# Kernel optimization log

Measured on AMD Instinct MI355X. Metric: run time of the kernel, lower is better.

The kernel has to match this reference:

```python
import jax, jax.numpy as jnp
import numpy as np

B, T, W, D = 4, 1000, 32, 200
ED, N, DCONV, DTR = 400, 16, 4, 13  # d_inner=2*d_model, d_state, d_conv, dt_rank=ceil(200/16)


def _causal_conv(x, w, b):
    # x: (B, L, ED), depthwise causal conv, kernel DCONV
    L = x.shape[1]
    xp = jnp.pad(x, ((0, 0), (DCONV - 1, 0), (0, 0)))
    y = sum(xp[:, k:k + L, :] * w[:, k] for k in range(DCONV))
    return y + b


def _ssm(x, A_log, Dp, xproj, dtw, dtb):
    # selective scan; x: (B, L, ED)
    A = -jnp.exp(A_log)                      # (ED, N)
    dbc = x @ xproj                          # (B, L, DTR+2N)
    delta, Bm, Cm = dbc[..., :DTR], dbc[..., DTR:DTR + N], dbc[..., DTR + N:]
    dt = jax.nn.softplus(delta @ dtw + dtb)  # (B, L, ED)
    dA = jnp.exp(dt[..., None] * A)                         # (B, L, ED, N)
    dBx = dt[..., None] * Bm[:, :, None, :] * x[..., None]  # (B, L, ED, N)

    def step(h, t):
        dA_t, dBx_t, C_t = t
        h = dA_t * h + dBx_t
        y = jnp.einsum('ben,bn->be', h, C_t)
        return h, y

    h0 = jnp.zeros((x.shape[0], ED, N), x.dtype)
    xs = (dA.transpose(1, 0, 2, 3), dBx.transpose(1, 0, 2, 3), Cm.transpose(1, 0, 2))
    _, ys = jax.lax.scan(step, h0, xs)
    return ys.transpose(1, 0, 2) + Dp * x


def _branch(x, in_proj, conv_w, conv_b, xproj, dtw, dtb, A_log, Dp):
    xz = x @ in_proj
    xp, z = xz[..., :ED], xz[..., ED:]
    xp = jax.nn.silu(_causal_conv(xp, conv_w, conv_b))
    y = _ssm(xp, A_log, Dp, xproj, dtw, dtb)
    return y * jax.nn.silu(z)


def setup_inputs() -> dict:
    key = jax.random.key(0)
    ks = jax.random.split(key, 24)
    s = 0.02
    nrm = lambda k, shape: jax.random.normal(k, shape, jnp.float32) * s
    inp = {}
    inp['input_ids'] = jax.random.normal(ks[0], (B, T, W, D), jnp.float32)
    inp['n_tweets'] = jax.random.randint(ks[1], (B,), 1, T + 1)
    inp['n_words'] = jax.random.randint(ks[2], (B, T), 1, W + 1)
    inp['cls_token'] = jnp.zeros((1, 1, D), jnp.float32)
    inp['w_attn'] = nrm(ks[3], (D, 1))
    inp['b_attn'] = jnp.zeros((1,), jnp.float32)
    inp['norm_w'] = jnp.ones((D,), jnp.float32)
    for i, d in enumerate(('f', 'b')):
        o = i * 8
        inp[f'in_proj_{d}'] = nrm(ks[4 + o], (D, 2 * ED))
        inp[f'conv_w_{d}'] = nrm(ks[5 + o], (ED, DCONV))
        inp[f'conv_b_{d}'] = jnp.zeros((ED,), jnp.float32)
        inp[f'xproj_{d}'] = nrm(ks[6 + o], (ED, DTR + 2 * N))
        inp[f'dtw_{d}'] = nrm(ks[7 + o], (DTR, ED))
        inp[f'dtb_{d}'] = jnp.zeros((ED,), jnp.float32)
        inp[f'A_log_{d}'] = jnp.log(jnp.broadcast_to(jnp.arange(1, N + 1, dtype=jnp.float32), (ED, N)))
        inp[f'D_{d}'] = jnp.ones((ED,), jnp.float32)
    inp['out_proj'] = nrm(ks[20], (ED, D))
    inp['head_w'] = nrm(ks[21], (D, 1))
    inp['head_b'] = jnp.zeros((1,), jnp.float32)
    return inp


def reference(input_ids, n_tweets, n_words, cls_token, w_attn, b_attn, norm_w,
              in_proj_f, conv_w_f, conv_b_f, xproj_f, dtw_f, dtb_f, A_log_f, D_f,
              in_proj_b, conv_w_b, conv_b_b, xproj_b, dtw_b, dtb_b, A_log_b, D_b,
              out_proj, head_w, head_b):
    Bz, Tz, Wz, Dz = input_ids.shape
    # ragged per-tweet attention pooling, fully vectorized with masks
    scores = jnp.squeeze(input_ids @ w_attn, -1) + b_attn[0]        # (B, T, W)
    wmask = jnp.arange(Wz) < n_words[..., None]                     # (B, T, W)
    scores = jnp.where(wmask, scores, -jnp.inf)
    attn = jax.nn.softmax(scores, axis=-1)
    tw = jnp.einsum('btw,btwd->btd', attn, input_ids)               # (B, T, D)
    tmask = jnp.arange(Tz) < n_tweets[:, None]
    tw = jnp.where(tmask[..., None], tw, 0.0)                       # padded tweets stay zero
    pos = Tz // 2
    x = jnp.concatenate([tw[:, :pos], jnp.broadcast_to(cls_token, (Bz, 1, Dz)), tw[:, pos:]], axis=1)
    # one bidirectional Mamba layer: pre-RMSNorm residual block
    xn = x * jax.lax.rsqrt(jnp.mean(x * x, axis=-1, keepdims=True) + 1e-5) * norm_w
    y_f = _branch(xn, in_proj_f, conv_w_f, conv_b_f, xproj_f, dtw_f, dtb_f, A_log_f, D_f)
    y_b = jnp.flip(_branch(jnp.flip(xn, 1), in_proj_b, conv_w_b, conv_b_b, xproj_b, dtw_b, dtb_b, A_log_b, D_b), 1)
    x = x + (y_f + y_b) @ out_proj
    logit = jnp.squeeze(x[:, pos] @ head_w, -1) + head_b[0]
    return jax.nn.sigmoid(logit)
```

## Files before the change

kernel.cpp:

```cpp
#include <hip/hip_runtime.h>
#include <cmath>

#define Bz 4
#define Tz 1000
#define Wz 32
#define Dz 200
#define EDz 400
#define Nz 16
#define DTRz 13
#define Lz 1001
#define POSz 500
#define LPz 501
#define TSTR 512
#define NEE 7
#define NZB 8
#define ZTOT 29728
#define NEG_BIG -1e30f

__device__ __forceinline__ float wave_sum(float v) {
#pragma unroll
  for (int o = 32; o; o >>= 1) v += __shfl_xor(v, o);
  return v;
}

__global__ __launch_bounds__(256) void k_front(
    const float* __restrict__ x, const int* __restrict__ n_tweets,
    const int* __restrict__ n_words, const float* __restrict__ w_attn,
    const float* __restrict__ b_attn, const float* __restrict__ norm_w,
    const float* __restrict__ cls, const float* __restrict__ out_proj,
    const float* __restrict__ head_w, const float* __restrict__ ipf,
    const float* __restrict__ ipb, float* __restrict__ xn,
    float* __restrict__ zbuf, float* __restrict__ vbuf,
    float* __restrict__ zero_base) {
  int bid = blockIdx.x;
  int tid = threadIdx.x;
  int wave = tid >> 6, lane = tid & 63;
  if (bid < 9) {
    if (bid == 0) {
      __shared__ float hw[Dz];
      if (tid < Dz) hw[tid] = head_w[tid];
      __syncthreads();
      for (int e = tid; e < EDz; e += 256) {
        float acc = 0.f;
        for (int d = 0; d < Dz; d += 4) {
          float4 ov = *(const float4*)(out_proj + e * Dz + d);
          acc += ov.x * hw[d] + ov.y * hw[d + 1] + ov.z * hw[d + 2] + ov.w * hw[d + 3];
        }
        vbuf[e] = acc;
      }
      return;
    }
    int id = bid - 1;
    int br = id >> 2, b = id & 3;
    __shared__ float xs[Dz];
    __shared__ float s_red[4];
    float val = (tid < Dz) ? cls[tid] : 0.f;
    float sq = wave_sum(val * val);
    if ((tid & 63) == 0) s_red[tid >> 6] = sq;
    __syncthreads();
    float tot = s_red[0] + s_red[1] + s_red[2] + s_red[3];
    float scale = rsqrtf(tot * (1.f / Dz) + 1e-5f);
    if (tid < Dz) {
      float o = val * scale * norm_w[tid];
      xs[tid] = o;
      if (br == 0) xn[((size_t)b * Lz + POSz) * Dz + tid] = o;
    }
    __syncthreads();
    const float* ip = br ? ipb : ipf;
    for (int e = tid; e < EDz; e += 256) {
      float acc = 0.f;
      for (int d = 0; d < Dz; ++d) acc += xs[d] * ip[d * (2 * EDz) + EDz + e];
      zbuf[((size_t)br * Bz + b) * EDz + e] = acc;
    }
    return;
  }
  if (bid < 9 + NZB) {
    int zb = bid - 9;
    float4* z = (float4*)zero_base;
    int per = ZTOT / NZB;
    for (int i = tid; i < per; i += 256)
      z[zb * per + i] = make_float4(0.f, 0.f, 0.f, 0.f);
    return;
  }
  int bt = (bid - 9 - NZB) * 4 + wave;
  int b = bt / Tz, t = bt - b * Tz;
  int l = (t < POSz) ? t : t + 1;
  float* outr = xn + ((size_t)b * Lz + l) * Dz;
  int ntw = n_tweets[b]; if (ntw > Tz) ntw = Tz;
  if (t >= ntw) {
    if (lane < 50) *(float4*)(outr + lane * 4) = make_float4(0.f, 0.f, 0.f, 0.f);
    return;
  }
  int nw = n_words[b * Tz + t]; if (nw > Wz) nw = Wz; if (nw < 1) nw = 1;
  const float* xs = x + ((size_t)(b * Tz + t)) * (Wz * Dz);
  int h = lane & 1, w = lane >> 1;
  float sc = 0.f;
  if (w < nw) {
    const float* xr = xs + w * Dz + h * 100;
    const float* wr = w_attn + h * 100;
#pragma unroll
    for (int i = 0; i < 25; ++i) {
      float4 xv = *(const float4*)(xr + i * 4);
      float4 wv = *(const float4*)(wr + i * 4);
      sc += xv.x * wv.x + xv.y * wv.y + xv.z * wv.z + xv.w * wv.w;
    }
  }
  sc += __shfl_xor(sc, 1);
  float scv = (w < nw) ? (sc + b_attn[0]) : NEG_BIG;
  float m = scv;
#pragma unroll
  for (int o = 32; o; o >>= 1) m = fmaxf(m, __shfl_xor(m, o));
  float en = __expf(scv - m);
  float es = (h == 0) ? en : 0.f;
  float tot = wave_sum(es);
  en /= tot;
  float4 val = make_float4(0.f, 0.f, 0.f, 0.f);
  const float* xc = xs + lane * 4;
  for (int ww = 0; ww < nw; ++ww) {
    float aw = __shfl(en, 2 * ww);
    if (lane < 50) {
      float4 xv = *(const float4*)(xc + ww * Dz);
      val.x += aw * xv.x; val.y += aw * xv.y;
      val.z += aw * xv.z; val.w += aw * xv.w;
    }
  }
  float sq = (lane < 50) ? (val.x * val.x + val.y * val.y + val.z * val.z + val.w * val.w) : 0.f;
  sq = wave_sum(sq);
  float scale = rsqrtf(sq * (1.f / Dz) + 1e-5f);
  if (lane < 50) {
    float4 nw4 = *(const float4*)(norm_w + lane * 4);
    float4 o = make_float4(val.x * scale * nw4.x, val.y * scale * nw4.y,
                           val.z * scale * nw4.z, val.w * scale * nw4.w);
    *(float4*)(outr + lane * 4) = o;
  }
}

__global__ __launch_bounds__(256) void k_gemmid(
    const float* __restrict__ xn,
    const float* __restrict__ ipf, const float* __restrict__ ipb,
    const float* __restrict__ cwf, const float* __restrict__ cwb,
    const float* __restrict__ cbf, const float* __restrict__ cbb,
    const float* __restrict__ xpjf, const float* __restrict__ xpjb,
    float* __restrict__ xp_t, float* __restrict__ dfin_g,
    float* __restrict__ Bm_t, float* __restrict__ Cend) {
  int bid = blockIdx.x;
  int ee = bid % NEE;
  int rem = bid / NEE;
  int tt = rem & 7, brb = rem >> 3;
  int br = brb >> 2, b = brb & 3;
  int t0 = tt * 64, e0 = ee * 64;
  int tid = threadIdx.x;
  int wave = tid >> 6, lane = tid & 63;
  const float* ip = br ? ipb : ipf;
  const float* cw = br ? cwb : cwf;
  const float* cb = br ? cbb : cbf;
  const float* xpj = br ? xpjb : xpjf;

  __shared__ float Xs[16][132];
  __shared__ float Ws[16][68];
  __shared__ float Pl[80][69];
  __shared__ float sred[4][64][45];

  int tx = tid & 15, ty = tid >> 4;

  const float* xr_[5];
  bool vr_[5];
  int colr_[5];
#pragma unroll
  for (int r = 0; r < 5; ++r) {
    int trow = r * 16 + ty;
    int t = t0 - 8 + trow;
    bool ok = (t >= 0 && t < LPz);
    int tc2 = ok ? t : 0;
    int l = br ? (Lz - 1 - tc2) : tc2;
    xr_[r] = xn + ((size_t)b * Lz + l) * Dz;
    vr_[r] = ok;
    colr_[r] = (trow / 5) * 8 + (trow % 5);
  }

  float acc[5][4];
#pragma unroll
  for (int i = 0; i < 5; ++i)
#pragma unroll
    for (int j = 0; j < 4; ++j) acc[i][j] = 0.f;

  float xv[5], wv[4];
#pragma unroll
  for (int r = 0; r < 5; ++r) xv[r] = vr_[r] ? xr_[r][tx] : 0.f;
#pragma unroll
  for (int c = 0; c < 4; ++c)
    wv[c] = ip[(size_t)ty * (2 * EDz) + e0 + tx * 4 + c];

  for (int it = 0; it < 13; ++it) {
    __syncthreads();
#pragma unroll
    for (int r = 0; r < 5; ++r) Xs[tx][colr_[r]] = xv[r];
#pragma unroll
    for (int c = 0; c < 4; ++c) Ws[ty][tx * 4 + c] = wv[c];
    __syncthreads();
    if (it < 12) {
      int dk = (it + 1) * 16;
      int d = dk + tx;
      bool dok = (d < Dz);
#pragma unroll
      for (int r = 0; r < 5; ++r)
        xv[r] = (vr_[r] && dok) ? xr_[r][d] : 0.f;
      int dw = dk + ty;
      bool wok = (dw < Dz);
#pragma unroll
      for (int c = 0; c < 4; ++c)
        wv[c] = wok ? ip[(size_t)dw * (2 * EDz) + e0 + tx * 4 + c] : 0.f;
    }
#pragma unroll
    for (int k = 0; k < 16; ++k) {
      float4 a4 = *(const float4*)&Xs[k][ty * 8];
      float a5 = Xs[k][ty * 8 + 4];
      float4 b4 = *(const float4*)&Ws[k][tx * 4];
      float av[5] = {a4.x, a4.y, a4.z, a4.w, a5};
      float bv[4] = {b4.x, b4.y, b4.z, b4.w};
#pragma unroll
      for (int i = 0; i < 5; ++i)
#pragma unroll
        for (int j = 0; j < 4; ++j) acc[i][j] += av[i] * bv[j];
    }
  }
  __syncthreads();
#pragma unroll
  for (int i = 0; i < 5; ++i)
#pragma unroll
    for (int j = 0; j < 4; ++j) Pl[ty * 5 + i][tx * 4 + j] = acc[i][j];
  __syncthreads();

  float accq[45];
#pragma unroll
  for (int q = 0; q < 45; ++q) accq[q] = 0.f;
  int t = t0 + lane;
#pragma unroll 2
  for (int i = 0; i < 16; ++i) {
    int e_loc = wave * 16 + i;
    int e = e0 + e_loc;
    if (e < EDz) {
      int row = lane + 8;
      float p0 = Pl[row - 3][e_loc];
      float p1 = Pl[row - 2][e_loc];
      float p2 = Pl[row - 1][e_loc];
      float p3 = Pl[row][e_loc];
      float4 c4 = *(const float4*)(cw + e * 4);
      float a = cb[e] + c4.x * p0 + c4.y * p1 + c4.z * p2 + c4.w * p3;
      float sp = a / (1.f + __expf(-a));
      xp_t[((size_t)brb * EDz + e) * TSTR + t] = sp;
      const float* xq = xpj + e * 45;
#pragma unroll
      for (int q = 0; q < 45; ++q) accq[q] += sp * xq[q];
    }
  }
#pragma unroll
  for (int q = 0; q < 45; ++q) sred[wave][lane][q] = accq[q];
  __syncthreads();
  if (wave < 2) {
#pragma unroll
    for (int q = 0; q < 45; ++q)
      sred[wave][lane][q] += sred[wave + 2][lane][q];
  }
  __syncthreads();
  if (wave == 0) {
#pragma unroll
    for (int q = 0; q < DTRz; ++q) {
      float v = sred[0][lane][q] + sred[1][lane][q];
      atomicAdd(&dfin_g[((size_t)brb * DTRz + q) * TSTR + t], v);
    }
#pragma unroll
    for (int n = 0; n < Nz; ++n) {
      float v = sred[0][lane][13 + n] + sred[1][lane][13 + n];
      atomicAdd(&Bm_t[((size_t)brb * Nz + n) * TSTR + t], v);
    }
    if (tt == 7 && lane == (POSz - 448)) {
#pragma unroll
      for (int n = 0; n < Nz; ++n) {
        float v = sred[0][lane][29 + n] + sred[1][lane][29 + n];
        atomicAdd(&Cend[brb * Nz + n], v);
      }
    }
  }
}

__global__ __launch_bounds__(512) void k_scan3(
    const float* __restrict__ xp_t, const float* __restrict__ dfin_g,
    const float* __restrict__ Bm_t, const float* __restrict__ Cend,
    const float* __restrict__ Alogf, const float* __restrict__ Alogb,
    const float* __restrict__ Dpf, const float* __restrict__ Dpb,
    const float* __restrict__ dtwf, const float* __restrict__ dtwb,
    const float* __restrict__ dtbf, const float* __restrict__ dtbb,
    const float* __restrict__ zbuf, const float* __restrict__ vbuf,
    float* __restrict__ ybuf) {
  int bid = blockIdx.x;
  int eg = bid % 50, brb = bid / 50;
  int br = brb >> 2;
  int tid = threadIdx.x;
  int wave = tid >> 6, lane = tid & 63;
  int e = eg * 8 + wave;

  __shared__ float sdf[DTRz * TSTR];
  __shared__ float sbm[Nz * TSTR];

  {
    const float4* src = (const float4*)(dfin_g + (size_t)brb * DTRz * TSTR);
    float4* dst = (float4*)sdf;
    for (int i = tid; i < DTRz * TSTR / 4; i += 512) dst[i] = src[i];
    const float4* src2 = (const float4*)(Bm_t + (size_t)brb * Nz * TSTR);
    float4* dst2 = (float4*)sbm;
    for (int i = tid; i < Nz * TSTR / 4; i += 512) dst2[i] = src2[i];
  }
  __syncthreads();

  const float* A_log = br ? Alogb : Alogf;
  const float* Dp = br ? Dpb : Dpf;
  const float* dtw = br ? dtwb : dtwf;
  const float* dtb = br ? dtbb : dtbf;
  float A[Nz];
  {
    const float4* ap = (const float4*)(A_log + e * Nz);
#pragma unroll
    for (int q = 0; q < 4; ++q) {
      float4 a4 = ap[q];
      A[q * 4 + 0] = -__expf(a4.x); A[q * 4 + 1] = -__expf(a4.y);
      A[q * 4 + 2] = -__expf(a4.z); A[q * 4 + 3] = -__expf(a4.w);
    }
  }
  float wq[DTRz];
#pragma unroll
  for (int q = 0; q < DTRz; ++q) wq[q] = dtw[q * EDz + e];
  float dtbe = dtb[e];
  const float* xpp = xp_t + ((size_t)brb * EDz + e) * TSTR;

  float dtt_r[8];
  float loc = 0.f;
#pragma unroll
  for (int c = 0; c < 8; ++c) {
    int t = c * 64 + lane;
    float s = dtbe;
#pragma unroll
    for (int q = 0; q < DTRz; ++q) s += sdf[q * TSTR + t] * wq[q];
    float dtv = (s > 20.f) ? s : log1pf(__expf(s));
    dtv = (t < LPz) ? dtv : 0.f;
    dtt_r[c] = dtv;
    loc += dtv;
  }
  float Stot = wave_sum(loc);
  float acc[Nz];
#pragma unroll
  for (int n = 0; n < Nz; ++n) acc[n] = 0.f;
  float carry = 0.f;
  for (int c = 0; c < 8; ++c) {
    int t = c * 64 + lane;
    bool act = t < LPz;
    float dtt = dtt_r[c];
    float xv = act ? xpp[t] : 0.f;
    float s = dtt;
#pragma unroll
    for (int o = 1; o < 64; o <<= 1) {
      float u = __shfl_up(s, o);
      s += (lane >= o) ? u : 0.f;
    }
    float S = carry + s;
    carry += __shfl(s, 63);
    float wt = dtt * xv;
    float decay = Stot - S;
#pragma unroll
    for (int n = 0; n < Nz; ++n) {
      float bv = act ? sbm[n * TSTR + t] : 0.f;
      acc[n] += __expf(A[n] * decay) * wt * bv;
    }
  }
#pragma unroll
  for (int o = 32; o; o >>= 1) {
#pragma unroll
    for (int n = 0; n < Nz; ++n) acc[n] += __shfl_xor(acc[n], o);
  }
  if (lane == 0) {
    float y = Dp[e] * xpp[LPz - 1];
#pragma unroll
    for (int n = 0; n < Nz; ++n) y += Cend[brb * Nz + n] * acc[n];
    float zz = zbuf[(size_t)brb * EDz + e];
    float sz = zz / (1.f + __expf(-zz));
    ybuf[(size_t)brb * EDz + e] = y * sz * vbuf[e];
  }
}

__global__ __launch_bounds__(256) void k_final(
    const float* __restrict__ cls, const float* __restrict__ head_w,
    const float* __restrict__ head_b, const float* __restrict__ ybuf,
    float* __restrict__ out) {
  int tid = threadIdx.x;
  int b = tid >> 6, lane = tid & 63;
  float acc = 0.f;
  for (int e = lane; e < EDz; e += 64)
    acc += ybuf[(size_t)b * EDz + e] + ybuf[(size_t)(Bz + b) * EDz + e];
  for (int d = lane; d < Dz; d += 64) acc += cls[d] * head_w[d];
  acc = wave_sum(acc);
  if (lane == 0) out[b] = 1.f / (1.f + __expf(-(acc + head_b[0])));
}

extern "C" void kernel_launch(void* const* d_in, const int* in_sizes, int n_in,
                              void* d_out, int out_size, void* d_ws, size_t ws_size,
                              hipStream_t stream) {
  const float* input_ids = (const float*)d_in[0];
  const int* n_tweets = (const int*)d_in[1];
  const int* n_words = (const int*)d_in[2];
  const float* cls = (const float*)d_in[3];
  const float* w_attn = (const float*)d_in[4];
  const float* b_attn = (const float*)d_in[5];
  const float* norm_w = (const float*)d_in[6];
  const float* ip[2] = {(const float*)d_in[7], (const float*)d_in[15]};
  const float* cw[2] = {(const float*)d_in[8], (const float*)d_in[16]};
  const float* cb[2] = {(const float*)d_in[9], (const float*)d_in[17]};
  const float* xpj[2] = {(const float*)d_in[10], (const float*)d_in[18]};
  const float* dtw[2] = {(const float*)d_in[11], (const float*)d_in[19]};
  const float* dtbp[2] = {(const float*)d_in[12], (const float*)d_in[20]};
  const float* Alog[2] = {(const float*)d_in[13], (const float*)d_in[21]};
  const float* Dpp[2] = {(const float*)d_in[14], (const float*)d_in[22]};
  const float* out_proj = (const float*)d_in[23];
  const float* head_w = (const float*)d_in[24];
  const float* head_b = (const float*)d_in[25];
  float* out = (float*)d_out;

  float* ws = (float*)d_ws;
  float* xn = ws;
  float* xp_t = xn + 800800;
  float* dfin = xp_t + 1638400;
  float* Bm_t = dfin + 53248;
  float* Cend = Bm_t + 65536;
  float* zbuf = Cend + 128;
  float* vbuf = zbuf + 3200;
  float* ybuf = vbuf + 400;

  hipLaunchKernelGGL(k_front, dim3(9 + NZB + Bz * Tz / 4), dim3(256), 0, stream,
                     input_ids, n_tweets, n_words, w_attn, b_attn, norm_w,
                     cls, out_proj, head_w, ip[0], ip[1], xn, zbuf, vbuf, dfin);
  hipLaunchKernelGGL(k_gemmid, dim3(2 * Bz * 8 * NEE), dim3(256), 0, stream,
                     xn, ip[0], ip[1], cw[0], cw[1], cb[0], cb[1],
                     xpj[0], xpj[1], xp_t, dfin, Bm_t, Cend);
  hipLaunchKernelGGL(k_scan3, dim3(2 * Bz * 50), dim3(512), 0, stream,
                     xp_t, dfin, Bm_t, Cend, Alog[0], Alog[1], Dpp[0], Dpp[1],
                     dtw[0], dtw[1], dtbp[0], dtbp[1], zbuf, vbuf, ybuf);
  hipLaunchKernelGGL(k_final, dim3(1), dim3(256), 0, stream,
                     cls, head_w, head_b, ybuf, out);
}
```

Measured before the change: 87.05 us.

## Widen GEMM K-tile to 25 with cooperative vectorized loads and shrink reduction smem

Reworks the in_proj GEMM tile loop in the conv/xproj kernel to use a K-step of 25 (8 iterations instead of 13), with a flattened cooperative load mapping and float4 weight loads. This cuts the number of barrier pairs and makes the global weight loads wider. The cross-wave reduction buffer is halved by having waves 2-3 add directly into the slots written by waves 0-1, which lowers LDS footprint and may allow higher occupancy. In exchange, each thread holds more registers for the prefetched loads.

```diff
diff --git a/kernel.cpp b/kernel.cpp
--- a/kernel.cpp
+++ b/kernel.cpp
@@ -156,26 +156,45 @@
   const float* cb = br ? cbb : cbf;
   const float* xpj = br ? xpjb : xpjf;
 
-  __shared__ float Xs[16][132];
-  __shared__ float Ws[16][68];
+  __shared__ float Xs[25][133];
+  __shared__ float Ws[25][68];
   __shared__ float Pl[80][69];
-  __shared__ float sred[4][64][45];
+  __shared__ float sred[2][64][45];
 
   int tx = tid & 15, ty = tid >> 4;
 
-  const float* xr_[5];
-  bool vr_[5];
-  int colr_[5];
-#pragma unroll
-  for (int r = 0; r < 5; ++r) {
-    int trow = r * 16 + ty;
-    int t = t0 - 8 + trow;
-    bool ok = (t >= 0 && t < LPz);
-    int tc2 = ok ? t : 0;
+  const float* xp_[8];
+  bool xok_[8], xw_[8];
+  int xk_[8], xcol_[8];
+#pragma unroll
+  for (int j = 0; j < 8; ++j) {
+    int idx = tid + 256 * j;
+    bool w = idx < 2000;
+    int iv = w ? idx : 0;
+    int row = iv / 25, k2 = iv - row * 25;
+    int t = t0 - 8 + row;
+    bool ok = w && (t >= 0) && (t < LPz);
+    int tc2 = (t >= 0 && t < LPz) ? t : 0;
     int l = br ? (Lz - 1 - tc2) : tc2;
-    xr_[r] = xn + ((size_t)b * Lz + l) * Dz;
-    vr_[r] = ok;
-    colr_[r] = (trow / 5) * 8 + (trow % 5);
+    xp_[j] = xn + ((size_t)b * Lz + l) * Dz + k2;
+    xok_[j] = ok;
+    xw_[j] = w;
+    xk_[j] = k2;
+    xcol_[j] = (row / 5) * 8 + (row % 5);
+  }
+  const float* wp_[2];
+  bool ww_[2];
+  int wk_[2], weq_[2];
+#pragma unroll
+  for (int i = 0; i < 2; ++i) {
+    int idx = tid + 256 * i;
+    bool w = idx < 400;
+    int iv = w ? idx : 0;
+    int k2 = iv >> 4, eq = iv & 15;
+    wp_[i] = ip + (size_t)k2 * (2 * EDz) + e0 + eq * 4;
+    ww_[i] = w;
+    wk_[i] = k2;
+    weq_[i] = eq;
   }
 
   float acc[5][4];
@@ -184,35 +203,35 @@
 #pragma unroll
     for (int j = 0; j < 4; ++j) acc[i][j] = 0.f;
 
-  float xv[5], wv[4];
-#pragma unroll
-  for (int r = 0; r < 5; ++r) xv[r] = vr_[r] ? xr_[r][tx] : 0.f;
-#pragma unroll
-  for (int c = 0; c < 4; ++c)
-    wv[c] = ip[(size_t)ty * (2 * EDz) + e0 + tx * 4 + c];
-
-  for (int it = 0; it < 13; ++it) {
+  float xsv[8];
+  float4 wsv[2];
+#pragma unroll
+  for (int j = 0; j < 8; ++j) xsv[j] = xok_[j] ? xp_[j][0] : 0.f;
+#pragma unroll
+  for (int i = 0; i < 2; ++i)
+    wsv[i] = ww_[i] ? *(const float4*)(wp_[i]) : make_float4(0.f, 0.f, 0.f, 0.f);
+
+  for (int it = 0; it < 8; ++it) {
     __syncthreads();
 #pragma unroll
-    for (int r = 0; r < 5; ++r) Xs[tx][colr_[r]] = xv[r];
-#pragma unroll
-    for (int c = 0; c < 4; ++c) Ws[ty][tx * 4 + c] = wv[c];
+    for (int j = 0; j < 8; ++j)
+      if (xw_[j]) Xs[xk_[j]][xcol_[j]] = xsv[j];
+#pragma unroll
+    for (int i = 0; i < 2; ++i)
+      if (ww_[i]) *(float4*)&Ws[wk_[i]][weq_[i] * 4] = wsv[i];
     __syncthreads();
-    if (it < 12) {
-      int dk = (it + 1) * 16;
-      int d = dk + tx;
-      bool dok = (d < Dz);
-#pragma unroll
-      for (int r = 0; r < 5; ++r)
-        xv[r] = (vr_[r] && dok) ? xr_[r][d] : 0.f;
-      int dw = dk + ty;
-      bool wok = (dw < Dz);
-#pragma unroll
-      for (int c = 0; c < 4; ++c)
-        wv[c] = wok ? ip[(size_t)dw * (2 * EDz) + e0 + tx * 4 + c] : 0.f;
-    }
-#pragma unroll
-    for (int k = 0; k < 16; ++k) {
+    if (it < 7) {
+      int dk = (it + 1) * 25;
+#pragma unroll
+      for (int j = 0; j < 8; ++j) xsv[j] = xok_[j] ? xp_[j][dk] : 0.f;
+      size_t woff = (size_t)dk * (2 * EDz);
+#pragma unroll
+      for (int i = 0; i < 2; ++i)
+        wsv[i] = ww_[i] ? *(const float4*)(wp_[i] + woff)
+                        : make_float4(0.f, 0.f, 0.f, 0.f);
+    }
+#pragma unroll
+    for (int k = 0; k < 25; ++k) {
       float4 a4 = *(const float4*)&Xs[k][ty * 8];
       float a5 = Xs[k][ty * 8 + 4];
       float4 b4 = *(const float4*)&Ws[k][tx * 4];
@@ -254,13 +273,14 @@
       for (int q = 0; q < 45; ++q) accq[q] += sp * xq[q];
     }
   }
-#pragma unroll
-  for (int q = 0; q < 45; ++q) sred[wave][lane][q] = accq[q];
+  if (wave < 2) {
+#pragma unroll
+    for (int q = 0; q < 45; ++q) sred[wave][lane][q] = accq[q];
+  }
   __syncthreads();
-  if (wave < 2) {
-#pragma unroll
-    for (int q = 0; q < 45; ++q)
-      sred[wave][lane][q] += sred[wave + 2][lane][q];
+  if (wave >= 2) {
+#pragma unroll
+    for (int q = 0; q < 45; ++q) sred[wave - 2][lane][q] += accq[q];
   }
   __syncthreads();
   if (wave == 0) {
```

After: 87.88 us. About the same (+1.0%).
